# Performance work log

Measured on AMD Instinct MI355X. Metric: run time of the kernel, lower is better.

Reference implementation:

```python
import jax, jax.numpy as jnp
import numpy as np

B, S, D, H = 2, 2048, 1024, 16
HD = D // H  # head_dim = 64


def setup_inputs() -> dict:
    key = jax.random.key(0)
    ks = jax.random.split(key, 12)
    s = 1.0 / np.sqrt(D)
    return {
        "q": jax.random.normal(ks[0], (B, S, D), jnp.float32),
        "k": jax.random.normal(ks[1], (B, S, D), jnp.float32),
        "v": jax.random.normal(ks[2], (B, S, D), jnp.float32),
        "mask": jnp.zeros((B, 1, 1, S), jnp.float32),
        "wq": jax.random.normal(ks[3], (D, D), jnp.float32) * s,
        "bq": jnp.zeros((D,), jnp.float32),
        "wk": jax.random.normal(ks[4], (D, D), jnp.float32) * s,
        "bk": jnp.zeros((D,), jnp.float32),
        "wv": jax.random.normal(ks[5], (D, D), jnp.float32) * s,
        "bv": jnp.zeros((D,), jnp.float32),
        "wo": jax.random.normal(ks[6], (D, D), jnp.float32) * s,
        "bo": jnp.zeros((D,), jnp.float32),
    }


def _split_heads(x):
    # [B, S, D] -> [B, H, S, HD]
    return x.reshape(B, S, H, HD).transpose(0, 2, 1, 3)


def reference(q, k, v, mask, wq, bq, wk, bk, wv, bv, wo, bo):
    _q = _split_heads(q @ wq + bq)
    _k = _split_heads(k @ wk + bk)
    _v = _split_heads(v @ wv + bv)
    scale = jnp.sqrt(jnp.float32(HD)) + 1e-8
    score = jnp.einsum("bhqd,bhkd->bhqk", _q, _k) / scale
    score = score + mask * -1e9
    attn = jax.nn.softmax(score, axis=-1)
    ctx = jnp.einsum("bhqk,bhkd->bhqd", attn, _v)
    ctx = ctx.transpose(0, 2, 1, 3).reshape(B, S, D)
    # dropout is identity at inference (training=False)
    return ctx @ wo + bo
```

## Files before the change

kernel.cpp:

```cpp
#include <hip/hip_runtime.h>
#include <hip/hip_bf16.h>

typedef unsigned short u16;
typedef __attribute__((ext_vector_type(8))) short s16x8;
typedef __attribute__((ext_vector_type(4))) short s16x4;
typedef __attribute__((ext_vector_type(4))) float f32x4;
typedef __attribute__((ext_vector_type(8))) unsigned short u16x8;
typedef __attribute__((ext_vector_type(4))) unsigned int u32x4;
typedef __attribute__((ext_vector_type(2))) unsigned int u32x2;

#define AS1(p) (const __attribute__((address_space(1))) void*)(p)
#define AS3(p) (__attribute__((address_space(3))) void*)(p)

__device__ __forceinline__ u16 f2bf(float f) {
  unsigned u = __builtin_bit_cast(unsigned, f);
  u += 0x7fffu + ((u >> 16) & 1u);
  return (u16)(u >> 16);
}

__device__ __forceinline__ unsigned cvtpk(float lo, float hi) {
  unsigned r;
  asm("v_cvt_pk_bf16_f32 %0, %1, %2" : "=v"(r) : "v"(lo), "v"(hi));
  return r;
}

__global__ __launch_bounds__(256) void prep(const float* __restrict__ q,
                                            const float* __restrict__ k,
                                            const float* __restrict__ v,
                                            const float* __restrict__ wq,
                                            const float* __restrict__ wk,
                                            const float* __restrict__ wv,
                                            const float* __restrict__ wo,
                                            u16* __restrict__ Xq, u16* __restrict__ Xk,
                                            u16* __restrict__ Xv, u16* __restrict__ Wqt,
                                            u16* __restrict__ Wkt, u16* __restrict__ Wvt,
                                            u16* __restrict__ Wot) {
  __shared__ float t[32][33];
  const int bid = blockIdx.x, tid = threadIdx.x;
  if (bid < 6144) {
    const int m = bid >> 11;
    const float* in = m == 0 ? q : m == 1 ? k : v;
    u16* out = m == 0 ? Xq : m == 1 ? Xk : Xv;
    const int i = ((bid & 2047) * 256 + tid) * 8;
    f32x4 a = *(const f32x4*)(in + i);
    f32x4 b = *(const f32x4*)(in + i + 4);
    u16x8 r;
    r[0] = f2bf(a[0]); r[1] = f2bf(a[1]); r[2] = f2bf(a[2]); r[3] = f2bf(a[3]);
    r[4] = f2bf(b[0]); r[5] = f2bf(b[1]); r[6] = f2bf(b[2]); r[7] = f2bf(b[3]);
    *(u16x8*)(out + i) = r;
  } else {
    const int b2 = bid - 6144;
    const int wsel = b2 >> 10;
    const float* w = wsel == 0 ? wq : wsel == 1 ? wk : wsel == 2 ? wv : wo;
    u16* wt = wsel == 0 ? Wqt : wsel == 1 ? Wkt : wsel == 2 ? Wvt : Wot;
    const int n0 = (b2 & 31) * 32, k0 = ((b2 >> 5) & 31) * 32;
    const int tx = tid & 31, ty = tid >> 5;
#pragma unroll
    for (int i = 0; i < 4; i++)
      t[ty + 8 * i][tx] = w[(size_t)(k0 + ty + 8 * i) * 1024 + n0 + tx];
    __syncthreads();
#pragma unroll
    for (int i = 0; i < 4; i++)
      wt[(size_t)(n0 + ty + 8 * i) * 1024 + k0 + tx] = f2bf(t[tx][ty + 8 * i]);
  }
}

__global__ __launch_bounds__(256) void gemm_qkv(const u16* __restrict__ Xq,
                                                const u16* __restrict__ Xk,
                                                const u16* __restrict__ Xv,
                                                const u16* __restrict__ Wqt,
                                                const u16* __restrict__ Wkt,
                                                const u16* __restrict__ Wvt,
                                                const float* __restrict__ bq,
                                                const float* __restrict__ bk,
                                                const float* __restrict__ bv,
                                                u16* __restrict__ Qb, u16* __restrict__ Kb,
                                                u16* __restrict__ Vt) {
  const int mode = blockIdx.z;
  const u16* A = mode == 0 ? Xq : mode == 1 ? Xk : Xv;
  const u16* Bt = mode == 0 ? Wqt : mode == 1 ? Wkt : Wvt;
  const float* bias = mode == 0 ? bq : mode == 1 ? bk : bv;
  u16* outp = mode == 0 ? Qb : mode == 1 ? Kb : Vt;

  __shared__ u16 Als[128 * 64];
  __shared__ u16 Bls[128 * 64];
  const int tid = threadIdx.x;
  const int lane = tid & 63;
  const int wid = tid >> 6;
  const int wm = wid >> 1, wn = wid & 1;
  const int m0 = blockIdx.y * 128, n0 = blockIdx.x * 128;
  const int g = lane >> 4, c = lane & 15;
  const int srl = lane >> 3, sch0 = lane & 7;
  f32x4 acc[4][4] = {};
  for (int kk = 0; kk < 1024; kk += 64) {
    __syncthreads();
#pragma unroll
    for (int j = 0; j < 4; j++) {
      const int rl = wid * 32 + j * 8 + srl;
      const int col = kk + ((sch0 ^ (rl & 7)) << 3);
      __builtin_amdgcn_global_load_lds(AS1(A + (size_t)(m0 + rl) * 1024 + col),
                                       AS3(&Als[(wid * 32 + j * 8) * 64]), 16, 0, 0);
      __builtin_amdgcn_global_load_lds(AS1(Bt + (size_t)(n0 + rl) * 1024 + col),
                                       AS3(&Bls[(wid * 32 + j * 8) * 64]), 16, 0, 0);
    }
    __syncthreads();
#pragma unroll
    for (int half = 0; half < 2; half++) {
      s16x8 af[4], bfr[4];
#pragma unroll
      for (int mi = 0; mi < 4; mi++) {
        const int r = wm * 64 + mi * 16 + c;
        af[mi] = *(const s16x8*)&Als[r * 64 + (((half * 4 + g) ^ (r & 7)) << 3)];
      }
#pragma unroll
      for (int ni = 0; ni < 4; ni++) {
        const int r = wn * 64 + ni * 16 + c;
        bfr[ni] = *(const s16x8*)&Bls[r * 64 + (((half * 4 + g) ^ (r & 7)) << 3)];
      }
      __builtin_amdgcn_s_setprio(1);
#pragma unroll
      for (int mi = 0; mi < 4; mi++)
#pragma unroll
        for (int ni = 0; ni < 4; ni++)
          acc[mi][ni] = __builtin_amdgcn_mfma_f32_16x16x32_bf16(af[mi], bfr[ni],
                                                                acc[mi][ni], 0, 0, 0);
      __builtin_amdgcn_s_setprio(0);
    }
  }
#pragma unroll
  for (int mi = 0; mi < 4; mi++) {
#pragma unroll
    for (int ni = 0; ni < 4; ni++) {
      const int gn = n0 + wn * 64 + ni * 16 + c;
      const float bb = bias[gn];
      const int gmb = m0 + wm * 64 + mi * 16 + (g << 2);
      const int hd = gn >> 6, d = gn & 63;
      if (mode == 2) {
        const int b = gmb >> 11, s0 = gmb & 2047;
        const int tile = s0 >> 6;
        const int jb = gmb & 63;
        const int j5b = jb & 31;
        const int posb = ((jb >> 5) << 5) + (((j5b & 15) >> 2) << 3) + ((j5b >> 4) << 2);
        s16x4 st;
#pragma unroll
        for (int r = 0; r < 4; r++) st[r] = (short)f2bf(acc[mi][ni][r] + bb);
        *(s16x4*)&Vt[(((size_t)b * 16 + hd) * 64 + d) * 2048 + tile * 64 + posb] = st;
      } else {
#pragma unroll
        for (int r = 0; r < 4; r++) {
          const int gm = gmb + r;
          float val = acc[mi][ni][r] + bb;
          const int b = gm >> 11, s = gm & 2047;
          if (mode == 0) val *= 0.18033688f;
          outp[(((size_t)b * 16 + hd) * 2048 + s) * 64 + d] = f2bf(val);
        }
      }
    }
  }
}

__global__ __launch_bounds__(256) void gemm_out(const u16* __restrict__ A,
                                                const u16* __restrict__ Bt,
                                                const float* __restrict__ bias,
                                                float* __restrict__ outp) {
  __shared__ u16 Als[128 * 64];
  __shared__ u16 Bls[64 * 64];
  const int tid = threadIdx.x;
  const int lane = tid & 63;
  const int wid = tid >> 6;
  const int m0 = blockIdx.y * 128, n0 = blockIdx.x * 64;
  const int g = lane >> 4, c = lane & 15;
  const int srl = lane >> 3, sch0 = lane & 7;
  f32x4 acc[2][4] = {};
  for (int kk = 0; kk < 1024; kk += 64) {
    __syncthreads();
#pragma unroll
    for (int j = 0; j < 4; j++) {
      const int rl = wid * 32 + j * 8 + srl;
      const int col = kk + ((sch0 ^ (rl & 7)) << 3);
      __builtin_amdgcn_global_load_lds(AS1(A + (size_t)(m0 + rl) * 1024 + col),
                                       AS3(&Als[(wid * 32 + j * 8) * 64]), 16, 0, 0);
    }
#pragma unroll
    for (int j = 0; j < 2; j++) {
      const int rl = wid * 16 + j * 8 + srl;
      const int col = kk + ((sch0 ^ (rl & 7)) << 3);
      __builtin_amdgcn_global_load_lds(AS1(Bt + (size_t)(n0 + rl) * 1024 + col),
                                       AS3(&Bls[(wid * 16 + j * 8) * 64]), 16, 0, 0);
    }
    __syncthreads();
#pragma unroll
    for (int half = 0; half < 2; half++) {
      s16x8 af[2], bfr[4];
#pragma unroll
      for (int mi = 0; mi < 2; mi++) {
        const int r = wid * 32 + mi * 16 + c;
        af[mi] = *(const s16x8*)&Als[r * 64 + (((half * 4 + g) ^ (r & 7)) << 3)];
      }
#pragma unroll
      for (int ni = 0; ni < 4; ni++) {
        const int r = ni * 16 + c;
        bfr[ni] = *(const s16x8*)&Bls[r * 64 + (((half * 4 + g) ^ (r & 7)) << 3)];
      }
      __builtin_amdgcn_s_setprio(1);
#pragma unroll
      for (int mi = 0; mi < 2; mi++)
#pragma unroll
        for (int ni = 0; ni < 4; ni++)
          acc[mi][ni] = __builtin_amdgcn_mfma_f32_16x16x32_bf16(af[mi], bfr[ni],
                                                                acc[mi][ni], 0, 0, 0);
      __builtin_amdgcn_s_setprio(0);
    }
  }
#pragma unroll
  for (int mi = 0; mi < 2; mi++) {
#pragma unroll
    for (int ni = 0; ni < 4; ni++) {
      const int gn = n0 + ni * 16 + c;
      const float bb = bias[gn];
      const int gmb = m0 + wid * 32 + mi * 16 + (g << 2);
#pragma unroll
      for (int r = 0; r < 4; r++)
        outp[(size_t)(gmb + r) * 1024 + gn] = acc[mi][ni][r] + bb;
    }
  }
}

__global__ __launch_bounds__(128) void attn_fwd(const u16* __restrict__ Qb,
                                                const u16* __restrict__ Kb,
                                                const u16* __restrict__ Vt,
                                                const float* __restrict__ mask,
                                                u16* __restrict__ ctx) {
  __shared__ u16 Kls[2][4096];
  __shared__ u16 Vls[2][4096];
  __shared__ float Mls[2048];
  const int tid = threadIdx.x;
  const int lane = tid & 63, wid = tid >> 6;
  const int n = blockIdx.x;
  const int bh = ((n & 7) << 2) | ((n >> 3) & 3);
  const int qblk = n >> 5;
  const int b = bh >> 4, hd = bh & 15;
  const int g = lane >> 4, c = lane & 15;
  const int qbase = qblk * 64 + wid * 32;

  const float* mp = mask + (size_t)b * 2048;
#pragma unroll
  for (int i = 0; i < 4; i++) {
    const int idx = (i * 128 + tid) * 4;
    f32x4 m4 = *(const f32x4*)(mp + idx);
    m4 *= -1.44269504e9f;
    *(f32x4*)&Mls[idx] = m4;
  }

  s16x8 qf[2][2];
#pragma unroll
  for (int sub = 0; sub < 2; sub++) {
    const u16* Qp = Qb + ((size_t)bh * 2048 + qbase + sub * 16 + c) * 64;
    qf[sub][0] = *(const s16x8*)(Qp + g * 8);
    qf[sub][1] = *(const s16x8*)(Qp + 32 + g * 8);
  }

  const u16* Kbh = Kb + (size_t)bh * 2048 * 64;
  const u16* Vbh = Vt + (size_t)bh * 64 * 2048;

  const int srl = lane >> 3;
  const int sch0 = lane & 7;
  auto STAGE = [&](int kv0, int bufi) {
#pragma unroll
    for (int j = 0; j < 4; j++) {
      const int rl = wid * 32 + j * 8 + srl;
      const int sch = sch0 ^ (rl & 7);
      __builtin_amdgcn_global_load_lds(AS1(Kbh + (size_t)(kv0 + rl) * 64 + sch * 8),
                                       AS3(&Kls[bufi][wid * 2048 + j * 512]), 16, 0, 0);
      __builtin_amdgcn_global_load_lds(AS1(Vbh + (size_t)rl * 2048 + kv0 + sch * 8),
                                       AS3(&Vls[bufi][wid * 2048 + j * 512]), 16, 0, 0);
    }
  };

  f32x4 o[2][4] = {};
  f32x4 ts2[2] = {};

  STAGE(0, 0);
  STAGE(64, 1);
  asm volatile("s_waitcnt lgkmcnt(0)" ::: "memory");

  for (int t = 0; t < 32; t++) {
    const int kv0 = t * 64;
    const int buf = t & 1;
    if (t < 31) {
      asm volatile("s_waitcnt vmcnt(8)" ::: "memory");
    } else {
      asm volatile("s_waitcnt vmcnt(0)" ::: "memory");
    }
    __builtin_amdgcn_sched_barrier(0);
    __builtin_amdgcn_s_barrier();
    __builtin_amdgcn_sched_barrier(0);

    f32x4 sacc[2][4] = {};
#pragma unroll
    for (int kvt = 0; kvt < 4; kvt++) {
      const int row = kvt * 16 + c;
      const int s7 = row & 7;
      const s16x8 kf0 = *(const s16x8*)&Kls[buf][row * 64 + ((g ^ s7) << 3)];
      const s16x8 kf1 = *(const s16x8*)&Kls[buf][row * 64 + (((4 + g) ^ s7) << 3)];
      sacc[0][kvt] = __builtin_amdgcn_mfma_f32_16x16x32_bf16(kf0, qf[0][0], sacc[0][kvt], 0, 0, 0);
      sacc[0][kvt] = __builtin_amdgcn_mfma_f32_16x16x32_bf16(kf1, qf[0][1], sacc[0][kvt], 0, 0, 0);
      sacc[1][kvt] = __builtin_amdgcn_mfma_f32_16x16x32_bf16(kf0, qf[1][0], sacc[1][kvt], 0, 0, 0);
      sacc[1][kvt] = __builtin_amdgcn_mfma_f32_16x16x32_bf16(kf1, qf[1][1], sacc[1][kvt], 0, 0, 0);
    }

    s16x8 vreg[4][2];
#pragma unroll
    for (int dblk = 0; dblk < 4; dblk++) {
      const int row = dblk * 16 + c;
      const int s7 = row & 7;
      const u16* base = &Vls[buf][row * 64];
      vreg[dblk][0] = *(const s16x8*)(base + ((g ^ s7) << 3));
      vreg[dblk][1] = *(const s16x8*)(base + (((4 + g) ^ s7) << 3));
    }
    asm volatile("s_waitcnt lgkmcnt(0)" ::: "memory");
    __builtin_amdgcn_sched_barrier(0);
    __builtin_amdgcn_s_barrier();
    __builtin_amdgcn_sched_barrier(0);
    if (t < 30) STAGE(kv0 + 128, buf);

    s16x8 pf[2][2];
#pragma unroll
    for (int qs = 0; qs < 2; qs++) {
      f32x4 p4[4];
#pragma unroll
      for (int kvt = 0; kvt < 4; kvt++) {
        const f32x4 mk = *(const f32x4*)&Mls[kv0 + kvt * 16 + 4 * g];
#pragma unroll
        for (int j = 0; j < 4; j++)
          p4[kvt][j] = __builtin_amdgcn_exp2f(sacc[qs][kvt][j] + mk[j]);
        ts2[qs] += p4[kvt];
      }
#pragma unroll
      for (int sub = 0; sub < 2; sub++) {
        u32x4 ww;
        ww[0] = cvtpk(p4[sub * 2][0], p4[sub * 2][1]);
        ww[1] = cvtpk(p4[sub * 2][2], p4[sub * 2][3]);
        ww[2] = cvtpk(p4[sub * 2 + 1][0], p4[sub * 2 + 1][1]);
        ww[3] = cvtpk(p4[sub * 2 + 1][2], p4[sub * 2 + 1][3]);
        pf[qs][sub] = __builtin_bit_cast(s16x8, ww);
      }
    }

#pragma unroll
    for (int dblk = 0; dblk < 4; dblk++)
#pragma unroll
      for (int subk = 0; subk < 2; subk++) {
        o[0][dblk] = __builtin_amdgcn_mfma_f32_16x16x32_bf16(vreg[dblk][subk], pf[0][subk], o[0][dblk], 0, 0, 0);
        o[1][dblk] = __builtin_amdgcn_mfma_f32_16x16x32_bf16(vreg[dblk][subk], pf[1][subk], o[1][dblk], 0, 0, 0);
      }
  }

#pragma unroll
  for (int qs = 0; qs < 2; qs++) {
    float ts = (ts2[qs][0] + ts2[qs][1]) + (ts2[qs][2] + ts2[qs][3]);
    ts += __shfl_xor(ts, 16);
    ts += __shfl_xor(ts, 32);
    const float inv = 1.0f / ts;
    u16* cp = ctx + ((size_t)b * 2048 + qbase + qs * 16 + c) * 1024 + hd * 64;
#pragma unroll
    for (int d = 0; d < 4; d++) {
      u32x2 st;
      st[0] = cvtpk(o[qs][d][0] * inv, o[qs][d][1] * inv);
      st[1] = cvtpk(o[qs][d][2] * inv, o[qs][d][3] * inv);
      *(u32x2*)&cp[d * 16 + 4 * g] = st;
    }
  }
}

extern "C" void kernel_launch(void* const* d_in, const int* in_sizes, int n_in,
                              void* d_out, int out_size, void* d_ws, size_t ws_size,
                              hipStream_t stream) {
  (void)in_sizes; (void)n_in; (void)out_size; (void)ws_size;
  const float* q = (const float*)d_in[0];
  const float* k = (const float*)d_in[1];
  const float* v = (const float*)d_in[2];
  const float* mask = (const float*)d_in[3];
  const float* wq = (const float*)d_in[4];
  const float* bq = (const float*)d_in[5];
  const float* wk = (const float*)d_in[6];
  const float* bk = (const float*)d_in[7];
  const float* wv = (const float*)d_in[8];
  const float* bv = (const float*)d_in[9];
  const float* wo = (const float*)d_in[10];
  const float* bo = (const float*)d_in[11];
  float* out = (float*)d_out;
  char* ws = (char*)d_ws;
  const size_t MB = (size_t)1 << 20;
  u16* Xq = (u16*)(ws + 0 * MB);
  u16* Xk = (u16*)(ws + 8 * MB);
  u16* Xv = (u16*)(ws + 16 * MB);
  u16* Wqt = (u16*)(ws + 24 * MB);
  u16* Wkt = (u16*)(ws + 26 * MB);
  u16* Wvt = (u16*)(ws + 28 * MB);
  u16* Wot = (u16*)(ws + 30 * MB);
  u16* Qb = (u16*)(ws + 32 * MB);
  u16* Kb = (u16*)(ws + 40 * MB);
  u16* Vt = (u16*)(ws + 48 * MB);
  u16* ctx = Xq;

  prep<<<10240, 256, 0, stream>>>(q, k, v, wq, wk, wv, wo, Xq, Xk, Xv, Wqt, Wkt, Wvt, Wot);
  gemm_qkv<<<dim3(8, 32, 3), 256, 0, stream>>>(Xq, Xk, Xv, Wqt, Wkt, Wvt, bq, bk, bv,
                                               Qb, Kb, Vt);
  attn_fwd<<<1024, 128, 0, stream>>>(Qb, Kb, Vt, mask, ctx);
  gemm_out<<<dim3(16, 32), 256, 0, stream>>>(ctx, Wot, bo, out);
}
```

Measured before the change: 137.2 us.

## Fuse fp32-to-bf16 activation conversion into QKV GEMM and skip all-zero mask

Removes the separate pass that converted q/k/v to bf16. The QKV GEMM now streams fp32 activations straight into LDS with an XOR swizzle and packs them to bf16 while reading MFMA fragments, which saves a full write and reread of the bf16 copies. It costs twice the LDS footprint and global traffic for the A tiles, plus conversion instructions inside the GEMM inner loop. The attention kernel also checks with a ballot whether the mask is all zero and, if so, skips the per-tile mask loads and adds. It also drops one lgkmcnt wait after the initial staging.

```diff
diff --git a/kernel.cpp b/kernel.cpp
--- a/kernel.cpp
+++ b/kernel.cpp
@@ -24,50 +24,31 @@
   return r;
 }
 
-__global__ __launch_bounds__(256) void prep(const float* __restrict__ q,
-                                            const float* __restrict__ k,
-                                            const float* __restrict__ v,
-                                            const float* __restrict__ wq,
-                                            const float* __restrict__ wk,
-                                            const float* __restrict__ wv,
-                                            const float* __restrict__ wo,
-                                            u16* __restrict__ Xq, u16* __restrict__ Xk,
-                                            u16* __restrict__ Xv, u16* __restrict__ Wqt,
-                                            u16* __restrict__ Wkt, u16* __restrict__ Wvt,
-                                            u16* __restrict__ Wot) {
+__global__ __launch_bounds__(256) void prep_w(const float* __restrict__ wq,
+                                              const float* __restrict__ wk,
+                                              const float* __restrict__ wv,
+                                              const float* __restrict__ wo,
+                                              u16* __restrict__ Wqt, u16* __restrict__ Wkt,
+                                              u16* __restrict__ Wvt, u16* __restrict__ Wot) {
   __shared__ float t[32][33];
-  const int bid = blockIdx.x, tid = threadIdx.x;
-  if (bid < 6144) {
-    const int m = bid >> 11;
-    const float* in = m == 0 ? q : m == 1 ? k : v;
-    u16* out = m == 0 ? Xq : m == 1 ? Xk : Xv;
-    const int i = ((bid & 2047) * 256 + tid) * 8;
-    f32x4 a = *(const f32x4*)(in + i);
-    f32x4 b = *(const f32x4*)(in + i + 4);
-    u16x8 r;
-    r[0] = f2bf(a[0]); r[1] = f2bf(a[1]); r[2] = f2bf(a[2]); r[3] = f2bf(a[3]);
-    r[4] = f2bf(b[0]); r[5] = f2bf(b[1]); r[6] = f2bf(b[2]); r[7] = f2bf(b[3]);
-    *(u16x8*)(out + i) = r;
-  } else {
-    const int b2 = bid - 6144;
-    const int wsel = b2 >> 10;
-    const float* w = wsel == 0 ? wq : wsel == 1 ? wk : wsel == 2 ? wv : wo;
-    u16* wt = wsel == 0 ? Wqt : wsel == 1 ? Wkt : wsel == 2 ? Wvt : Wot;
-    const int n0 = (b2 & 31) * 32, k0 = ((b2 >> 5) & 31) * 32;
-    const int tx = tid & 31, ty = tid >> 5;
-#pragma unroll
-    for (int i = 0; i < 4; i++)
-      t[ty + 8 * i][tx] = w[(size_t)(k0 + ty + 8 * i) * 1024 + n0 + tx];
-    __syncthreads();
-#pragma unroll
-    for (int i = 0; i < 4; i++)
-      wt[(size_t)(n0 + ty + 8 * i) * 1024 + k0 + tx] = f2bf(t[tx][ty + 8 * i]);
-  }
-}
-
-__global__ __launch_bounds__(256) void gemm_qkv(const u16* __restrict__ Xq,
-                                                const u16* __restrict__ Xk,
-                                                const u16* __restrict__ Xv,
+  const int b2 = blockIdx.x, tid = threadIdx.x;
+  const int wsel = b2 >> 10;
+  const float* w = wsel == 0 ? wq : wsel == 1 ? wk : wsel == 2 ? wv : wo;
+  u16* wt = wsel == 0 ? Wqt : wsel == 1 ? Wkt : wsel == 2 ? Wvt : Wot;
+  const int n0 = (b2 & 31) * 32, k0 = ((b2 >> 5) & 31) * 32;
+  const int tx = tid & 31, ty = tid >> 5;
+#pragma unroll
+  for (int i = 0; i < 4; i++)
+    t[ty + 8 * i][tx] = w[(size_t)(k0 + ty + 8 * i) * 1024 + n0 + tx];
+  __syncthreads();
+#pragma unroll
+  for (int i = 0; i < 4; i++)
+    wt[(size_t)(n0 + ty + 8 * i) * 1024 + k0 + tx] = f2bf(t[tx][ty + 8 * i]);
+}
+
+__global__ __launch_bounds__(256) void gemm_qkv(const float* __restrict__ Aq,
+                                                const float* __restrict__ Ak,
+                                                const float* __restrict__ Av,
                                                 const u16* __restrict__ Wqt,
                                                 const u16* __restrict__ Wkt,
                                                 const u16* __restrict__ Wvt,
@@ -77,12 +58,12 @@
                                                 u16* __restrict__ Qb, u16* __restrict__ Kb,
                                                 u16* __restrict__ Vt) {
   const int mode = blockIdx.z;
-  const u16* A = mode == 0 ? Xq : mode == 1 ? Xk : Xv;
+  const float* A = mode == 0 ? Aq : mode == 1 ? Ak : Av;
   const u16* Bt = mode == 0 ? Wqt : mode == 1 ? Wkt : Wvt;
   const float* bias = mode == 0 ? bq : mode == 1 ? bk : bv;
   u16* outp = mode == 0 ? Qb : mode == 1 ? Kb : Vt;
 
-  __shared__ u16 Als[128 * 64];
+  __shared__ float AlsF[128 * 64];
   __shared__ u16 Bls[128 * 64];
   const int tid = threadIdx.x;
   const int lane = tid & 63;
@@ -91,15 +72,21 @@
   const int m0 = blockIdx.y * 128, n0 = blockIdx.x * 128;
   const int g = lane >> 4, c = lane & 15;
   const int srl = lane >> 3, sch0 = lane & 7;
+  const int arl = lane >> 4, ac15 = lane & 15;
   f32x4 acc[4][4] = {};
   for (int kk = 0; kk < 1024; kk += 64) {
     __syncthreads();
 #pragma unroll
+    for (int j = 0; j < 8; j++) {
+      const int rl = wid * 32 + j * 4 + arl;
+      const int scol = kk + ((ac15 ^ (rl & 15)) << 2);
+      __builtin_amdgcn_global_load_lds(AS1(A + (size_t)(m0 + rl) * 1024 + scol),
+                                       AS3(&AlsF[(wid * 32 + j * 4) * 64]), 16, 0, 0);
+    }
+#pragma unroll
     for (int j = 0; j < 4; j++) {
       const int rl = wid * 32 + j * 8 + srl;
       const int col = kk + ((sch0 ^ (rl & 7)) << 3);
-      __builtin_amdgcn_global_load_lds(AS1(A + (size_t)(m0 + rl) * 1024 + col),
-                                       AS3(&Als[(wid * 32 + j * 8) * 64]), 16, 0, 0);
       __builtin_amdgcn_global_load_lds(AS1(Bt + (size_t)(n0 + rl) * 1024 + col),
                                        AS3(&Bls[(wid * 32 + j * 8) * 64]), 16, 0, 0);
     }
@@ -110,7 +97,15 @@
 #pragma unroll
       for (int mi = 0; mi < 4; mi++) {
         const int r = wm * 64 + mi * 16 + c;
-        af[mi] = *(const s16x8*)&Als[r * 64 + (((half * 4 + g) ^ (r & 7)) << 3)];
+        const int j2 = (half * 4 + g) * 2;
+        const f32x4 a0 = *(const f32x4*)&AlsF[r * 64 + ((j2 ^ (r & 15)) << 2)];
+        const f32x4 a1 = *(const f32x4*)&AlsF[r * 64 + (((j2 + 1) ^ (r & 15)) << 2)];
+        u32x4 ww;
+        ww[0] = cvtpk(a0[0], a0[1]);
+        ww[1] = cvtpk(a0[2], a0[3]);
+        ww[2] = cvtpk(a1[0], a1[1]);
+        ww[3] = cvtpk(a1[2], a1[3]);
+        af[mi] = __builtin_bit_cast(s16x8, ww);
       }
 #pragma unroll
       for (int ni = 0; ni < 4; ni++) {
@@ -234,6 +229,7 @@
   __shared__ u16 Kls[2][4096];
   __shared__ u16 Vls[2][4096];
   __shared__ float Mls[2048];
+  __shared__ int mfl[2];
   const int tid = threadIdx.x;
   const int lane = tid & 63, wid = tid >> 6;
   const int n = blockIdx.x;
@@ -244,13 +240,21 @@
   const int qbase = qblk * 64 + wid * 32;
 
   const float* mp = mask + (size_t)b * 2048;
+  int th_any = 0;
 #pragma unroll
   for (int i = 0; i < 4; i++) {
     const int idx = (i * 128 + tid) * 4;
     f32x4 m4 = *(const f32x4*)(mp + idx);
+    th_any |= (m4[0] != 0.f) | (m4[1] != 0.f) | (m4[2] != 0.f) | (m4[3] != 0.f);
     m4 *= -1.44269504e9f;
     *(f32x4*)&Mls[idx] = m4;
   }
+  {
+    unsigned long long bal = __ballot(th_any);
+    if (lane == 0) mfl[wid] = (bal != 0ULL);
+  }
+  __syncthreads();
+  const int havemask = __builtin_amdgcn_readfirstlane(mfl[0] | mfl[1]);
 
   s16x8 qf[2][2];
 #pragma unroll
@@ -282,7 +286,6 @@
 
   STAGE(0, 0);
   STAGE(64, 1);
-  asm volatile("s_waitcnt lgkmcnt(0)" ::: "memory");
 
   for (int t = 0; t < 32; t++) {
     const int kv0 = t * 64;
@@ -328,13 +331,23 @@
 #pragma unroll
     for (int qs = 0; qs < 2; qs++) {
       f32x4 p4[4];
-#pragma unroll
-      for (int kvt = 0; kvt < 4; kvt++) {
-        const f32x4 mk = *(const f32x4*)&Mls[kv0 + kvt * 16 + 4 * g];
-#pragma unroll
-        for (int j = 0; j < 4; j++)
-          p4[kvt][j] = __builtin_amdgcn_exp2f(sacc[qs][kvt][j] + mk[j]);
-        ts2[qs] += p4[kvt];
+      if (!havemask) {
+#pragma unroll
+        for (int kvt = 0; kvt < 4; kvt++) {
+#pragma unroll
+          for (int j = 0; j < 4; j++)
+            p4[kvt][j] = __builtin_amdgcn_exp2f(sacc[qs][kvt][j]);
+          ts2[qs] += p4[kvt];
+        }
+      } else {
+#pragma unroll
+        for (int kvt = 0; kvt < 4; kvt++) {
+          const f32x4 mk = *(const f32x4*)&Mls[kv0 + kvt * 16 + 4 * g];
+#pragma unroll
+          for (int j = 0; j < 4; j++)
+            p4[kvt][j] = __builtin_amdgcn_exp2f(sacc[qs][kvt][j] + mk[j]);
+          ts2[qs] += p4[kvt];
+        }
       }
 #pragma unroll
       for (int sub = 0; sub < 2; sub++) {
@@ -392,9 +405,7 @@
   float* out = (float*)d_out;
   char* ws = (char*)d_ws;
   const size_t MB = (size_t)1 << 20;
-  u16* Xq = (u16*)(ws + 0 * MB);
-  u16* Xk = (u16*)(ws + 8 * MB);
-  u16* Xv = (u16*)(ws + 16 * MB);
+  u16* ctx = (u16*)(ws + 0 * MB);
   u16* Wqt = (u16*)(ws + 24 * MB);
   u16* Wkt = (u16*)(ws + 26 * MB);
   u16* Wvt = (u16*)(ws + 28 * MB);
@@ -402,10 +413,9 @@
   u16* Qb = (u16*)(ws + 32 * MB);
   u16* Kb = (u16*)(ws + 40 * MB);
   u16* Vt = (u16*)(ws + 48 * MB);
-  u16* ctx = Xq;
-
-  prep<<<10240, 256, 0, stream>>>(q, k, v, wq, wk, wv, wo, Xq, Xk, Xv, Wqt, Wkt, Wvt, Wot);
-  gemm_qkv<<<dim3(8, 32, 3), 256, 0, stream>>>(Xq, Xk, Xv, Wqt, Wkt, Wvt, bq, bk, bv,
+
+  prep_w<<<4096, 256, 0, stream>>>(wq, wk, wv, wo, Wqt, Wkt, Wvt, Wot);
+  gemm_qkv<<<dim3(8, 32, 3), 256, 0, stream>>>(q, k, v, Wqt, Wkt, Wvt, bq, bk, bv,
                                                Qb, Kb, Vt);
   attn_fwd<<<1024, 128, 0, stream>>>(Qb, Kb, Vt, mask, ctx);
   gemm_out<<<dim3(16, 32), 256, 0, stream>>>(ctx, Wot, bo, out);
```

New measurement: 174.6 us. +27.2%, slower.
